# Kernel tuning notes

Measured on AMD Instinct MI355X. Metric: run time of the kernel, lower is better.

The kernel has to match this reference:

```python
import jax, jax.numpy as jnp
import numpy as np

HIDDEN_DIM = 512
SCALE = float(np.sqrt(HIDDEN_DIM))  # hidden_dim ** 0.5, matches torch


def setup_inputs() -> dict:
    key = jax.random.key(0)
    ks = jax.random.split(key, 4)
    B, S, D_IN = 8, 4096, 64
    x = jax.random.normal(ks[0], (B, S, D_IN), dtype=jnp.float32)
    # Linear weights stored as [in, out] (transposed vs torch's [out, in])
    Wq = jax.random.normal(ks[1], (D_IN, HIDDEN_DIM), dtype=jnp.float32) * (1.0 / np.sqrt(D_IN))
    Wk = jax.random.normal(ks[2], (D_IN, HIDDEN_DIM), dtype=jnp.float32) * (1.0 / np.sqrt(D_IN))
    Wv = jax.random.normal(ks[3], (D_IN, HIDDEN_DIM), dtype=jnp.float32) * (1.0 / np.sqrt(D_IN))
    bq = jnp.zeros((HIDDEN_DIM,), dtype=jnp.float32)
    bk = jnp.zeros((HIDDEN_DIM,), dtype=jnp.float32)
    bv = jnp.zeros((HIDDEN_DIM,), dtype=jnp.float32)
    return {"x": x, "Wq": Wq, "bq": bq, "Wk": Wk, "bk": bk, "Wv": Wv, "bv": bv}


def reference(x, Wq, bq, Wk, bk, Wv, bv):
    # Q/K/V projections: [B, S, H]
    Q = jnp.einsum('bsd,dh->bsh', x, Wq) + bq
    K = jnp.einsum('bsd,dh->bsh', x, Wk) + bk
    V = jnp.einsum('bsd,dh->bsh', x, Wv) + bv
    # Naive single-head attention with full [B, S, S] score matrix,
    # matching the original torch math exactly.
    scores = jnp.einsum('bqh,bkh->bqk', Q, K) / SCALE
    attn = jax.nn.softmax(scores, axis=-1)
    return jnp.einsum('bqk,bkh->bqh', attn, V)
```

## Files before the change

kernel.cpp:

```cpp
#include <hip/hip_runtime.h>
#include <hip/hip_bf16.h>
#include <math.h>


#define SS 4096
#define DD 64
#define HH 512

#define CSCALE ((float)(1.4426950408889634 * 0.04419417382415922))

typedef __bf16 bf16x8 __attribute__((ext_vector_type(8)));
typedef float  f32x4  __attribute__((ext_vector_type(4)));
typedef float  f32x16 __attribute__((ext_vector_type(16)));
typedef unsigned int u32x4 __attribute__((ext_vector_type(4)));

__device__ __forceinline__ float b2f(__hip_bfloat16 v) { return __bfloat162float(v); }

__device__ __forceinline__ f32x4 mfma16(bf16x8 a, bf16x8 b, f32x4 c) {
  return __builtin_amdgcn_mfma_f32_16x16x32_bf16(a, b, c, 0, 0, 0);
}
__device__ __forceinline__ f32x16 mfma32(bf16x8 a, bf16x8 b, f32x16 c) {
  return __builtin_amdgcn_mfma_f32_32x32x16_bf16(a, b, c, 0, 0, 0);
}

__device__ __forceinline__ unsigned pack2(float a, float b) {
  float2 f2; f2.x = a; f2.y = b;
  __hip_bfloat162 h2 = __float22bfloat162_rn(f2);
  unsigned u; __builtin_memcpy(&u, &h2, 4);
  return u;
}

__device__ __forceinline__ float loadf(const void* p, size_t i, int isF32) {
  return isF32 ? ((const float*)p)[i] : b2f(((const __hip_bfloat16*)p)[i]);
}
__device__ __forceinline__ void load8f(const void* p, size_t i, int isF32, float* o) {
  if (isF32) {
    const float4 a = *(const float4*)((const float*)p + i);
    const float4 b = *(const float4*)((const float*)p + i + 4);
    o[0]=a.x; o[1]=a.y; o[2]=a.z; o[3]=a.w; o[4]=b.x; o[5]=b.y; o[6]=b.z; o[7]=b.w;
  } else {
    const bf16x8 v = *(const bf16x8*)((const __hip_bfloat16*)p + i);
#pragma unroll
    for (int k = 0; k < 8; ++k) { __hip_bfloat16 h; __builtin_memcpy(&h, ((const unsigned short*)&v) + k, 2); o[k] = b2f(h); }
  }
}

__global__ void dtype_probe(const void* __restrict__ Wq, int* __restrict__ flag) {
  const unsigned short* h = (const unsigned short*)Wq;
  const int lane = threadIdx.x;
  unsigned int bits = ((unsigned int)h[lane * 2]) << 16;
  float v; __builtin_memcpy(&v, &bits, 4);
  v = fabsf(v);
  if (!isfinite(v) || v > 1e10f) v = 1e10f;
  for (int off = 1; off < 64; off <<= 1) v = fmaxf(v, __shfl_xor(v, off, 64));
  if (lane == 0) *flag = (v > 1e6f) ? 1 : 0;
}

__global__ __launch_bounds__(256) void prep_kernel(
    const void* __restrict__ Wq, const void* __restrict__ Wk,
    const void* __restrict__ Wv, const void* __restrict__ bq,
    const void* __restrict__ bk, __hip_bfloat16* __restrict__ MT,
    float* __restrict__ u, float* __restrict__ w_, float* __restrict__ c_,
    __hip_bfloat16* __restrict__ wvT, const int* __restrict__ flag) {
  const int t = threadIdx.x, blk = blockIdx.x;
  const int isF32 = *flag;
  if (blk < 64) {
    __shared__ float red[256];
    const int i = blk, j = t >> 2, part = t & 3;
    float acc = 0.f, aq[8], ak[8];
    for (int c = 0; c < 16; ++c) {
      load8f(Wq, (size_t)i * HH + part * 128 + c * 8, isF32, aq);
      load8f(Wk, (size_t)j * HH + part * 128 + c * 8, isF32, ak);
#pragma unroll
      for (int k = 0; k < 8; ++k) acc = fmaf(aq[k], ak[k], acc);
    }
    red[t] = acc;
    __syncthreads();
    if (t < 64)
      MT[t * 64 + i] = __float2bfloat16(red[t*4] + red[t*4+1] + red[t*4+2] + red[t*4+3]);
  } else if (blk == 64) {
    __shared__ float pu[256], pw[256], pc[64];
    const int i = t & 63, part = t >> 6;
    float au = 0.f, aw = 0.f, v1[8], v2[8];
    for (int c = 0; c < 16; ++c) {
      load8f(Wq, (size_t)i * HH + part * 128 + c * 8, isF32, v1);
      load8f(bk, part * 128 + c * 8, isF32, v2);
#pragma unroll
      for (int k = 0; k < 8; ++k) au = fmaf(v1[k], v2[k], au);
      load8f(Wk, (size_t)i * HH + part * 128 + c * 8, isF32, v1);
      load8f(bq, part * 128 + c * 8, isF32, v2);
#pragma unroll
      for (int k = 0; k < 8; ++k) aw = fmaf(v1[k], v2[k], aw);
    }
    pu[t] = au; pw[t] = aw;
    if (t < 64) {
      float s = 0.f;
      for (int e = 0; e < 8; ++e)
        s = fmaf(loadf(bq, t * 8 + e, isF32), loadf(bk, t * 8 + e, isF32), s);
      pc[t] = s;
    }
    __syncthreads();
    if (t < 64) {
      u[t]  = pu[t] + pu[t+64] + pu[t+128] + pu[t+192];
      w_[t] = pw[t] + pw[t+64] + pw[t+128] + pw[t+192];
    }
    if (t == 0) {
      float s = 0.f;
      for (int e = 0; e < 64; ++e) s += pc[e];
      *c_ = s;
    }
  } else {
    const int base = (blk - 65) * 2048 + t;
    for (int r = 0; r < 8; ++r) {
      const int e = base + r * 256;
      const int h = e >> 6, d = e & 63;
      wvT[e] = __float2bfloat16(loadf(Wv, (size_t)d * HH + h, isF32));
    }
  }
}

__global__ __launch_bounds__(256) void proj_kernel(
    const void* __restrict__ xraw, const __hip_bfloat16* __restrict__ MT,
    const float* __restrict__ u, const float* __restrict__ w_,
    const float* __restrict__ c_, __hip_bfloat16* __restrict__ xc,
    __hip_bfloat16* __restrict__ y, float* __restrict__ qb,
    float* __restrict__ kb, __hip_bfloat16* __restrict__ xT,
    const int* __restrict__ flag) {
  __shared__ __hip_bfloat16 xs[64 * 72];
  __shared__ __hip_bfloat16 Ms[64 * 72];
  __shared__ float us[64], wl[64];
  __shared__ float cs;

  const int t = threadIdx.x;
  const int isF32 = *flag;
  {
    const int r = t >> 2, cb = (t & 3) * 16;
    *(bf16x8*)(&Ms[r * 72 + cb])     = *(const bf16x8*)(MT + r * 64 + cb);
    *(bf16x8*)(&Ms[r * 72 + cb + 8]) = *(const bf16x8*)(MT + r * 64 + cb + 8);
  }
  if (t < 64) { us[t] = u[t]; wl[t] = w_[t]; }
  if (t == 0) cs = *c_;

  const int b = blockIdx.x & 7;
  const int sbase = (blockIdx.x >> 3) * 64;
  const int rbase = b * SS + sbase;

  for (int i = 0; i < 2; ++i) {
    const int e = i * 256 + t;
    const int row = e >> 3, col = (e & 7) * 8;
    float v[8];
    load8f(xraw, (size_t)(rbase + row) * DD + col, isF32, v);
    __hip_bfloat16* dp = xs + row * 72 + col;
#pragma unroll
    for (int k = 0; k < 8; ++k) dp[k] = __float2bfloat16(v[k]);
  }
  __syncthreads();

  const int wv = t >> 6, lane = t & 63;
  const int l16 = lane & 15, quad = lane >> 4;
  const bf16x8 A0 = *(const bf16x8*)(&xs[(wv * 16 + l16) * 72 + quad * 8]);
  const bf16x8 A1 = *(const bf16x8*)(&xs[(wv * 16 + l16) * 72 + 32 + quad * 8]);
#pragma unroll
  for (int nt = 0; nt < 4; ++nt) {
    const bf16x8 B0 = *(const bf16x8*)(&Ms[(nt * 16 + l16) * 72 + quad * 8]);
    const bf16x8 B1 = *(const bf16x8*)(&Ms[(nt * 16 + l16) * 72 + 32 + quad * 8]);
    f32x4 C = (f32x4){0.f, 0.f, 0.f, 0.f};
    C = mfma16(A0, B0, C);
    C = mfma16(A1, B1, C);
#pragma unroll
    for (int r = 0; r < 4; ++r)
      y[(size_t)(rbase + wv * 16 + quad * 4 + r) * DD + nt * 16 + l16] =
          __float2bfloat16(C[r]);
  }
  if (t < 64) {
    float qa = 0.f, ka = 0.f;
    for (int d = 0; d < 64; ++d) {
      const float xv = b2f(xs[t * 72 + d]);
      qa = fmaf(xv, us[d], qa);
      ka = fmaf(xv, wl[d], ka);
    }
    qb[rbase + t] = (qa + cs) * CSCALE;
    kb[rbase + t] = ka * CSCALE;
  }
  for (int i = 0; i < 2; ++i) {
    const int e = i * 256 + t;
    const int row = e >> 3, col = (e & 7) * 8;
    *(bf16x8*)(xc + (size_t)(rbase + row) * DD + col) = *(const bf16x8*)(xs + row * 72 + col);
  }
  for (int i = 0; i < 16; ++i) {
    const int d = i * 4 + (t >> 6);
    const int sl = t & 63;
    xT[((size_t)b * DD + d) * SS + sbase + sl] = xs[sl * 72 + d];
  }
}

__global__ __launch_bounds__(256) void attn_split(
    const __hip_bfloat16* __restrict__ x,
    const __hip_bfloat16* __restrict__ y,
    const float* __restrict__ qb, const float* __restrict__ kb,
    const __hip_bfloat16* __restrict__ xT,
    float* __restrict__ Opart, float* __restrict__ lpart, int lgs) {
  __shared__ __hip_bfloat16 xs[2][32 * 72];
  __shared__ __hip_bfloat16 vsm[2][64 * 40];
  const int tid = threadIdx.x;
  const int wv = tid >> 6, lane = tid & 63;
  const int l32 = lane & 31, hi = lane >> 5;
  const int b = blockIdx.x & 7;
  const int nspl = 1 << lgs;
  const int ks = (blockIdx.x >> 3) & (nspl - 1);
  const int qg = blockIdx.x >> (3 + lgs);
  const int kspl = SS >> lgs;
  const int koff = ks * kspl;
  const size_t rowq = ((size_t)b << 12) + (size_t)qg * 128 + wv * 32;

  bf16x8 Y[4];
#pragma unroll
  for (int mi = 0; mi < 4; ++mi)
    Y[mi] = *(const bf16x8*)(y + (rowq + l32) * DD + mi * 16 + hi * 8);
  const float qbl = qb[rowq + l32];

  const int sxr = tid >> 3, sxc = (tid & 7) * 8;
  const int g = sxr >> 2;
  const int taur = (sxr & 3) + 4 * ((g & 4) | ((g & 1) << 1) | ((g >> 1) & 1));
  const int svd = tid >> 2, svc = (tid & 3) * 8;
  const __hip_bfloat16* gx = x + ((size_t)b * SS + koff + sxr) * DD + sxc;
  const __hip_bfloat16* gv = xT + ((size_t)b * DD + svd) * SS + koff + svc;
  const float* kbp = kb + (size_t)b * SS + koff + hi * 8;

  bf16x8 nx = *(const bf16x8*)gx;
  bf16x8 nv = *(const bf16x8*)gv;
  *(bf16x8*)(&xs[0][taur * 72 + sxc]) = nx;
  *(bf16x8*)(&vsm[0][svd * 40 + svc]) = nv;
  nx = *(const bf16x8*)(gx + 32 * DD);
  nv = *(const bf16x8*)(gv + 32);
  __syncthreads();

  f32x16 O0, O1;
#pragma unroll
  for (int r = 0; r < 16; ++r) { O0[r] = 0.f; O1[r] = 0.f; }
  float lp = 0.f;

  for (int kt = 0; kt < kspl; kt += 32) {
    const int p = (kt >> 5) & 1, np = p ^ 1;
    if (kt + 32 < kspl) {
      *(bf16x8*)(&xs[np][taur * 72 + sxc]) = nx;
      *(bf16x8*)(&vsm[np][svd * 40 + svc]) = nv;
      if (kt + 64 < kspl) {
        nx = *(const bf16x8*)(gx + (size_t)(kt + 64) * DD);
        nv = *(const bf16x8*)(gv + (kt + 64));
      }
    }
    const f32x4 kb0a = *(const f32x4*)(kbp + kt);
    const f32x4 kb0b = *(const f32x4*)(kbp + kt + 4);
    const f32x4 kb1a = *(const f32x4*)(kbp + kt + 16);
    const f32x4 kb1b = *(const f32x4*)(kbp + kt + 20);

    const bf16x8 A0 = *(const bf16x8*)(&xs[p][l32 * 72 + hi * 8]);
    const bf16x8 A1 = *(const bf16x8*)(&xs[p][l32 * 72 + 16 + hi * 8]);
    const bf16x8 A2 = *(const bf16x8*)(&xs[p][l32 * 72 + 32 + hi * 8]);
    const bf16x8 A3 = *(const bf16x8*)(&xs[p][l32 * 72 + 48 + hi * 8]);

    f32x16 S;
#pragma unroll
    for (int r = 0; r < 16; ++r) S[r] = 0.f;
    S = mfma32(A0, Y[0], S);
    S = mfma32(A1, Y[1], S);
    S = mfma32(A2, Y[2], S);
    S = mfma32(A3, Y[3], S);

    float pv[16];
#pragma unroll
    for (int r = 0; r < 16; ++r) {
      const float kv = (r < 4) ? kb0a[r & 3]
                     : (r < 8) ? kb0b[r & 3]
                     : (r < 12) ? kb1a[r & 3] : kb1b[r & 3];
      pv[r] = __builtin_amdgcn_exp2f(fmaf(S[r], CSCALE, qbl + kv));
    }
    {
      float s0 = (pv[0]+pv[1]) + (pv[2]+pv[3]);
      float s1 = (pv[4]+pv[5]) + (pv[6]+pv[7]);
      float s2 = (pv[8]+pv[9]) + (pv[10]+pv[11]);
      float s3 = (pv[12]+pv[13]) + (pv[14]+pv[15]);
      lp += (s0 + s1) + (s2 + s3);
    }
    u32x4 R0, R1;
    R0[0] = pack2(pv[0], pv[1]);  R0[1] = pack2(pv[2], pv[3]);
    R0[2] = pack2(pv[4], pv[5]);  R0[3] = pack2(pv[6], pv[7]);
    R1[0] = pack2(pv[8], pv[9]);  R1[1] = pack2(pv[10], pv[11]);
    R1[2] = pack2(pv[12], pv[13]); R1[3] = pack2(pv[14], pv[15]);
    bf16x8 Pf0, Pf1;
    __builtin_memcpy(&Pf0, &R0, 16);
    __builtin_memcpy(&Pf1, &R1, 16);

    const bf16x8 V00 = *(const bf16x8*)(&vsm[p][l32 * 40 + hi * 8]);
    const bf16x8 V10 = *(const bf16x8*)(&vsm[p][l32 * 40 + 16 + hi * 8]);
    const bf16x8 V01 = *(const bf16x8*)(&vsm[p][(l32 + 32) * 40 + hi * 8]);
    const bf16x8 V11 = *(const bf16x8*)(&vsm[p][(l32 + 32) * 40 + 16 + hi * 8]);

    O0 = mfma32(Pf0, V00, O0);
    O0 = mfma32(Pf1, V10, O0);
    O1 = mfma32(Pf0, V01, O1);
    O1 = mfma32(Pf1, V11, O1);

    __syncthreads();
  }

  lp += __shfl_xor(lp, 32, 64);
  const size_t NP = (size_t)SS * 8;
  if (hi == 0) lpart[(size_t)ks * NP + rowq + l32] = lp;

  float* Op = Opart + ((size_t)ks * NP + rowq) * 64;
#pragma unroll
  for (int r = 0; r < 16; ++r) {
    const int qrow = (r & 3) + 8 * (r >> 2) + 4 * hi;
    Op[(size_t)qrow * 64 + l32]      = O0[r];
    Op[(size_t)qrow * 64 + 32 + l32] = O1[r];
  }
}

__global__ __launch_bounds__(128) void combine_kernel(
    const float* __restrict__ Opart, const float* __restrict__ lpart,
    const __hip_bfloat16* __restrict__ wvT, const void* __restrict__ bv_raw,
    void* __restrict__ out_raw, const int* __restrict__ flag, int nspl) {
  const int tid = threadIdx.x;
  const int wv = tid >> 6, lane = tid & 63;
  const int l16 = lane & 15, quad = lane >> 4;
  const size_t q0 = (size_t)blockIdx.x * 32 + (size_t)wv * 16;
  const int isF32 = *flag;
  const size_t NP = (size_t)SS * 8;

  float lsum = 0.f;
  for (int s = 0; s < nspl; ++s) lsum += lpart[(size_t)s * NP + q0 + l16];
  const float linv = (lsum > 0.f) ? 1.0f / lsum : 0.f;

  float vlo[8], vhi[8];
#pragma unroll
  for (int j = 0; j < 8; ++j) { vlo[j] = 0.f; vhi[j] = 0.f; }
  for (int s = 0; s < nspl; ++s) {
    const float* p0 = Opart + ((size_t)s * NP + q0 + l16) * 64 + quad * 8;
#pragma unroll
    for (int j = 0; j < 8; j += 4) {
      const float4 a = *(const float4*)(p0 + j);
      vlo[j]   += a.x; vlo[j+1] += a.y; vlo[j+2] += a.z; vlo[j+3] += a.w;
      const float4 c = *(const float4*)(p0 + 32 + j);
      vhi[j]   += c.x; vhi[j+1] += c.y; vhi[j+2] += c.z; vhi[j+3] += c.w;
    }
  }
  u32x4 Rlo, Rhi;
#pragma unroll
  for (int j = 0; j < 4; ++j) {
    Rlo[j] = pack2(vlo[2*j] * linv, vlo[2*j+1] * linv);
    Rhi[j] = pack2(vhi[2*j] * linv, vhi[2*j+1] * linv);
  }
  bf16x8 Alo, Ahi;
  __builtin_memcpy(&Alo, &Rlo, 16);
  __builtin_memcpy(&Ahi, &Rhi, 16);

  float* outf = (float*)out_raw;
  __hip_bfloat16* outb = (__hip_bfloat16*)out_raw;
#pragma unroll 4
  for (int ht = 0; ht < 32; ++ht) {
    const __hip_bfloat16* wp = wvT + (size_t)(ht * 16 + l16) * DD + quad * 8;
    const bf16x8 Wlo = *(const bf16x8*)wp;
    const bf16x8 Whi = *(const bf16x8*)(wp + 32);
    f32x4 C = (f32x4){0.f, 0.f, 0.f, 0.f};
    C = mfma16(Alo, Wlo, C);
    C = mfma16(Ahi, Whi, C);
    const float bvv = loadf(bv_raw, ht * 16 + l16, isF32);
#pragma unroll
    for (int r = 0; r < 4; ++r) {
      const size_t oidx = (q0 + quad * 4 + r) * HH + ht * 16 + l16;
      const float val = C[r] + bvv;
      if (isF32) outf[oidx] = val;
      else       outb[oidx] = __float2bfloat16(val);
    }
  }
}

__global__ __launch_bounds__(256) void attn_kernel(
    const __hip_bfloat16* __restrict__ x,
    const __hip_bfloat16* __restrict__ y,
    const float* __restrict__ qb, const float* __restrict__ kb,
    const __hip_bfloat16* __restrict__ xT,
    const __hip_bfloat16* __restrict__ wvT,
    const void* __restrict__ bv_raw,
    void* __restrict__ out_raw, const int* __restrict__ flag) {
  __shared__ __hip_bfloat16 xs[2][32 * 72];
  __shared__ __hip_bfloat16 vsm[2][64 * 40];
  __shared__ float kbl[SS];
  const int tid = threadIdx.x;
  const int wv = tid >> 6, lane = tid & 63;
  const int l16 = lane & 15, quad = lane >> 4;
  const int b = blockIdx.x & 7;
  const int qt = (blockIdx.x >> 3) * 4 + wv;
  const size_t rowq = ((size_t)b << 12) + ((size_t)qt << 4);
  const int isF32 = *flag;

  const __hip_bfloat16* xb  = x  + ((size_t)b * SS) * DD;
  const __hip_bfloat16* xTb = xT + ((size_t)b * DD) * SS;
  const float* kbb = kb + ((size_t)b * SS);

  const __hip_bfloat16* yp = y + (rowq + l16) * DD + quad * 8;
  const bf16x8 Ylo = *(const bf16x8*)yp;
  const bf16x8 Yhi = *(const bf16x8*)(yp + 32);
  const float qbl = qb[rowq + l16];

  const int sxr = tid >> 3, sxc = (tid & 7) * 8;
  const int taur = (sxr & 3) + ((sxr >> 3) << 2) + (((sxr >> 2) & 1) << 4);
  const int svd = tid >> 2, svc = (tid & 3) * 8;
  const __hip_bfloat16* gx = xb + (size_t)sxr * DD + sxc;
  const __hip_bfloat16* gv = xTb + (size_t)svd * SS + svc;

#pragma unroll
  for (int j = 0; j < 4; ++j) {
    const int c = j * 256 + tid;
    *(f32x4*)(&kbl[c * 4]) = *(const f32x4*)(kbb + c * 4);
  }

  bf16x8 nx = *(const bf16x8*)gx;
  bf16x8 nv = *(const bf16x8*)gv;
  *(bf16x8*)(&xs[0][taur * 72 + sxc]) = nx;
  *(bf16x8*)(&vsm[0][svd * 40 + svc]) = nv;
  nx = *(const bf16x8*)(gx + 32 * DD);
  nv = *(const bf16x8*)(gv + 32);
  __syncthreads();

  bf16x8 onesb;
#pragma unroll
  for (int j = 0; j < 8; ++j) onesb[j] = (__bf16)1.0f;

  f32x4 O[4];
#pragma unroll
  for (int n = 0; n < 4; ++n) O[n] = (f32x4){0.f, 0.f, 0.f, 0.f};
  f32x4 Ol = (f32x4){0.f, 0.f, 0.f, 0.f};

  for (int kt = 0; kt < SS; kt += 32) {
    const int p = (kt >> 5) & 1, np = p ^ 1;
    if (kt + 32 < SS) {
      *(bf16x8*)(&xs[np][taur * 72 + sxc]) = nx;
      *(bf16x8*)(&vsm[np][svd * 40 + svc]) = nv;
      if (kt + 64 < SS) {
        nx = *(const bf16x8*)(gx + (size_t)(kt + 64) * DD);
        nv = *(const bf16x8*)(gv + (kt + 64));
      }
    }
    const bf16x8 B00 = *(const bf16x8*)(&xs[p][l16 * 72 + quad * 8]);
    const bf16x8 B01 = *(const bf16x8*)(&xs[p][l16 * 72 + 32 + quad * 8]);
    const bf16x8 B10 = *(const bf16x8*)(&xs[p][(16 + l16) * 72 + quad * 8]);
    const bf16x8 B11 = *(const bf16x8*)(&xs[p][(16 + l16) * 72 + 32 + quad * 8]);
    const bf16x8 V0 = *(const bf16x8*)(&vsm[p][l16 * 40 + quad * 8]);
    const bf16x8 V1 = *(const bf16x8*)(&vsm[p][(16 + l16) * 40 + quad * 8]);
    const bf16x8 V2 = *(const bf16x8*)(&vsm[p][(32 + l16) * 40 + quad * 8]);
    const bf16x8 V3 = *(const bf16x8*)(&vsm[p][(48 + l16) * 40 + quad * 8]);

    f32x4 S0 = (f32x4){0.f, 0.f, 0.f, 0.f};
    f32x4 S1 = (f32x4){0.f, 0.f, 0.f, 0.f};
    S0 = mfma16(B00, Ylo, S0);
    S0 = mfma16(B01, Yhi, S0);
    S1 = mfma16(B10, Ylo, S1);
    S1 = mfma16(B11, Yhi, S1);

    const f32x4 kb0 = *(const f32x4*)(&kbl[kt + quad * 8]);
    const f32x4 kb1 = *(const f32x4*)(&kbl[kt + quad * 8 + 4]);

    float p0[4], p1[4];
#pragma unroll
    for (int r = 0; r < 4; ++r) {
      p0[r] = __builtin_amdgcn_exp2f(fmaf(S0[r], CSCALE, qbl + kb0[r]));
      p1[r] = __builtin_amdgcn_exp2f(fmaf(S1[r], CSCALE, qbl + kb1[r]));
    }
    u32x4 R;
    R[0] = pack2(p0[0], p0[1]);
    R[1] = pack2(p0[2], p0[3]);
    R[2] = pack2(p1[0], p1[1]);
    R[3] = pack2(p1[2], p1[3]);
    bf16x8 Pf;
    __builtin_memcpy(&Pf, &R, 16);

    O[0] = mfma16(Pf, V0, O[0]);
    O[1] = mfma16(Pf, V1, O[1]);
    O[2] = mfma16(Pf, V2, O[2]);
    O[3] = mfma16(Pf, V3, O[3]);
    Ol = mfma16(Pf, onesb, Ol);

    __syncthreads();
  }

  float inv_l[4];
#pragma unroll
  for (int r = 0; r < 4; ++r)
    inv_l[r] = (Ol[r] > 0.f) ? 1.0f / Ol[r] : 0.f;
  __hip_bfloat16* pl = &xs[0][0] + wv * 1152;
#pragma unroll
  for (int n = 0; n < 4; ++n)
#pragma unroll
    for (int r = 0; r < 4; ++r) {
      const int row = quad * 4 + r;
      pl[row * 72 + n * 16 + l16] = __float2bfloat16(O[n][r] * inv_l[r]);
    }
  __syncthreads();
  const bf16x8 Alo = *(const bf16x8*)(pl + l16 * 72 + quad * 8);
  const bf16x8 Ahi = *(const bf16x8*)(pl + l16 * 72 + 32 + quad * 8);

  float* outf = (float*)out_raw;
  __hip_bfloat16* outb = (__hip_bfloat16*)out_raw;
#pragma unroll 4
  for (int ht = 0; ht < 32; ++ht) {
    const __hip_bfloat16* wp = wvT + (size_t)(ht * 16 + l16) * DD + quad * 8;
    const bf16x8 Wlo = *(const bf16x8*)wp;
    const bf16x8 Whi = *(const bf16x8*)(wp + 32);
    f32x4 C = (f32x4){0.f, 0.f, 0.f, 0.f};
    C = mfma16(Alo, Wlo, C);
    C = mfma16(Ahi, Whi, C);
    const float bvv = loadf(bv_raw, ht * 16 + l16, isF32);
#pragma unroll
    for (int r = 0; r < 4; ++r) {
      const size_t oidx = (rowq + quad * 4 + r) * HH + ht * 16 + l16;
      const float val = C[r] + bvv;
      if (isF32) outf[oidx] = val;
      else       outb[oidx] = __float2bfloat16(val);
    }
  }
}

extern "C" void kernel_launch(void* const* d_in, const int* in_sizes, int n_in,
                              void* d_out, int out_size, void* d_ws,
                              size_t ws_size, hipStream_t stream) {
  char* ws = (char*)d_ws;
  int*   flag = (int*)(ws + 0);
  __hip_bfloat16* MT = (__hip_bfloat16*)(ws + 1024);
  float* u    = (float*)(ws + 9216);
  float* w_   = (float*)(ws + 9728);
  float* c_   = (float*)(ws + 10240);
  __hip_bfloat16* wvT = (__hip_bfloat16*)(ws + 32768);
  __hip_bfloat16* xc  = (__hip_bfloat16*)(ws + 131072);
  __hip_bfloat16* y   = (__hip_bfloat16*)(ws + 4325376);
  float* qb = (float*)(ws + 8519680);
  float* kb = (float*)(ws + 8650752);
  __hip_bfloat16* xT = (__hip_bfloat16*)(ws + 8781824);
  float* Opart = (float*)(ws + 16777216);
  const size_t NP = (size_t)SS * 8;
  const size_t need4 = 16777216UL + 4UL * NP * 64 * 4 + 4UL * NP * 4;
  const size_t need2 = 16777216UL + 2UL * NP * 64 * 4 + 2UL * NP * 4;

  dtype_probe<<<1, 64, 0, stream>>>(d_in[1], flag);
  prep_kernel<<<81, 256, 0, stream>>>(d_in[1], d_in[3], d_in[5], d_in[2],
                                      d_in[4], MT, u, w_, c_, wvT, flag);
  proj_kernel<<<512, 256, 0, stream>>>(d_in[0], MT, u, w_, c_, xc, y, qb, kb,
                                       xT, flag);
  if (ws_size >= need4) {
    float* lpart = (float*)(ws + 16777216 + 4UL * NP * 64 * 4);
    attn_split<<<1024, 256, 0, stream>>>(xc, y, qb, kb, xT, Opart, lpart, 2);
    combine_kernel<<<1024, 128, 0, stream>>>(Opart, lpart, wvT, d_in[6], d_out,
                                             flag, 4);
  } else if (ws_size >= need2) {
    float* lpart = (float*)(ws + 16777216 + 2UL * NP * 64 * 4);
    attn_split<<<512, 256, 0, stream>>>(xc, y, qb, kb, xT, Opart, lpart, 1);
    combine_kernel<<<1024, 128, 0, stream>>>(Opart, lpart, wvT, d_in[6], d_out,
                                             flag, 2);
  } else {
    attn_kernel<<<512, 256, 0, stream>>>(xc, y, qb, kb, xT, wvT, d_in[6],
                                         d_out, flag);
  }
}
```

Baseline: 193.0 us.

## Fuse split-K combine and V projection into attention via last-block atomic counter

Replaces the separate combine kernel with a last-arriving-block scheme inside the split attention kernel. Each query group's four key-split blocks bump an atomic counter, and the last one sums the partial O and l values, normalizes them, and runs the Wv projection with bias straight to the output. The counters are zeroed in proj_kernel. This removes a kernel launch and its tail, but leaves the final projection to only a quarter of the blocks and adds fences and atomics.

```diff
diff --git a/kernel.cpp b/kernel.cpp
--- a/kernel.cpp
+++ b/kernel.cpp
@@ -125,7 +125,7 @@
     const float* __restrict__ c_, __hip_bfloat16* __restrict__ xc,
     __hip_bfloat16* __restrict__ y, float* __restrict__ qb,
     float* __restrict__ kb, __hip_bfloat16* __restrict__ xT,
-    const int* __restrict__ flag) {
+    int* __restrict__ cnt, const int* __restrict__ flag) {
   __shared__ __hip_bfloat16 xs[64 * 72];
   __shared__ __hip_bfloat16 Ms[64 * 72];
   __shared__ float us[64], wl[64];
@@ -133,6 +133,7 @@
 
   const int t = threadIdx.x;
   const int isF32 = *flag;
+  if (blockIdx.x == 0 && t < 256) cnt[t] = 0;
   {
     const int r = t >> 2, cb = (t & 3) * 16;
     *(bf16x8*)(&Ms[r * 72 + cb])     = *(const bf16x8*)(MT + r * 64 + cb);
@@ -191,6 +192,196 @@
     const int d = i * 4 + (t >> 6);
     const int sl = t & 63;
     xT[((size_t)b * DD + d) * SS + sbase + sl] = xs[sl * 72 + d];
+  }
+}
+
+__global__ __launch_bounds__(256) void attn_split_fused(
+    const __hip_bfloat16* __restrict__ x,
+    const __hip_bfloat16* __restrict__ y,
+    const float* __restrict__ qb, const float* __restrict__ kb,
+    const __hip_bfloat16* __restrict__ xT,
+    float* __restrict__ Opart, float* __restrict__ lpart,
+    int* __restrict__ cnt,
+    const __hip_bfloat16* __restrict__ wvT, const void* __restrict__ bv_raw,
+    void* __restrict__ out_raw, const int* __restrict__ flag) {
+  __shared__ __hip_bfloat16 xs[2][32 * 72];
+  __shared__ __hip_bfloat16 vsm[2][64 * 40];
+  __shared__ int lastflag;
+  const int tid = threadIdx.x;
+  const int wv = tid >> 6, lane = tid & 63;
+  const int l32 = lane & 31, hi = lane >> 5;
+  const int b = blockIdx.x & 7;
+  const int ks = (blockIdx.x >> 3) & 3;
+  const int qg = blockIdx.x >> 5;
+  const int kspl = SS >> 2;
+  const int koff = ks * kspl;
+  const size_t rowq = ((size_t)b << 12) + ((size_t)(qg & 31)) * 128 + wv * 32;
+  const size_t NP = (size_t)SS * 8;
+
+  bf16x8 Y[4];
+#pragma unroll
+  for (int mi = 0; mi < 4; ++mi)
+    Y[mi] = *(const bf16x8*)(y + (rowq + l32) * DD + mi * 16 + hi * 8);
+  const float qbl = qb[rowq + l32];
+
+  const int sxr = tid >> 3, sxc = (tid & 7) * 8;
+  const int g = sxr >> 2;
+  const int taur = (sxr & 3) + 4 * ((g & 4) | ((g & 1) << 1) | ((g >> 1) & 1));
+  const int svd = tid >> 2, svc = (tid & 3) * 8;
+  const __hip_bfloat16* gx = x + ((size_t)b * SS + koff + sxr) * DD + sxc;
+  const __hip_bfloat16* gv = xT + ((size_t)b * DD + svd) * SS + koff + svc;
+  const float* kbp = kb + (size_t)b * SS + koff + hi * 8;
+
+  bf16x8 nx = *(const bf16x8*)gx;
+  bf16x8 nv = *(const bf16x8*)gv;
+  *(bf16x8*)(&xs[0][taur * 72 + sxc]) = nx;
+  *(bf16x8*)(&vsm[0][svd * 40 + svc]) = nv;
+  nx = *(const bf16x8*)(gx + 32 * DD);
+  nv = *(const bf16x8*)(gv + 32);
+  __syncthreads();
+
+  f32x16 O0, O1;
+#pragma unroll
+  for (int r = 0; r < 16; ++r) { O0[r] = 0.f; O1[r] = 0.f; }
+  float lp = 0.f;
+
+  for (int kt = 0; kt < kspl; kt += 32) {
+    const int p = (kt >> 5) & 1, np = p ^ 1;
+    if (kt + 32 < kspl) {
+      *(bf16x8*)(&xs[np][taur * 72 + sxc]) = nx;
+      *(bf16x8*)(&vsm[np][svd * 40 + svc]) = nv;
+      if (kt + 64 < kspl) {
+        nx = *(const bf16x8*)(gx + (size_t)(kt + 64) * DD);
+        nv = *(const bf16x8*)(gv + (kt + 64));
+      }
+    }
+    const f32x4 kb0a = *(const f32x4*)(kbp + kt);
+    const f32x4 kb0b = *(const f32x4*)(kbp + kt + 4);
+    const f32x4 kb1a = *(const f32x4*)(kbp + kt + 16);
+    const f32x4 kb1b = *(const f32x4*)(kbp + kt + 20);
+
+    const bf16x8 A0 = *(const bf16x8*)(&xs[p][l32 * 72 + hi * 8]);
+    const bf16x8 A1 = *(const bf16x8*)(&xs[p][l32 * 72 + 16 + hi * 8]);
+    const bf16x8 A2 = *(const bf16x8*)(&xs[p][l32 * 72 + 32 + hi * 8]);
+    const bf16x8 A3 = *(const bf16x8*)(&xs[p][l32 * 72 + 48 + hi * 8]);
+
+    f32x16 S;
+#pragma unroll
+    for (int r = 0; r < 16; ++r) S[r] = 0.f;
+    S = mfma32(A0, Y[0], S);
+    S = mfma32(A1, Y[1], S);
+    S = mfma32(A2, Y[2], S);
+    S = mfma32(A3, Y[3], S);
+
+    float pv[16];
+#pragma unroll
+    for (int r = 0; r < 16; ++r) {
+      const float kv = (r < 4) ? kb0a[r & 3]
+                     : (r < 8) ? kb0b[r & 3]
+                     : (r < 12) ? kb1a[r & 3] : kb1b[r & 3];
+      pv[r] = __builtin_amdgcn_exp2f(fmaf(S[r], CSCALE, qbl + kv));
+    }
+    {
+      float s0 = (pv[0]+pv[1]) + (pv[2]+pv[3]);
+      float s1 = (pv[4]+pv[5]) + (pv[6]+pv[7]);
+      float s2 = (pv[8]+pv[9]) + (pv[10]+pv[11]);
+      float s3 = (pv[12]+pv[13]) + (pv[14]+pv[15]);
+      lp += (s0 + s1) + (s2 + s3);
+    }
+    u32x4 R0, R1;
+    R0[0] = pack2(pv[0], pv[1]);  R0[1] = pack2(pv[2], pv[3]);
+    R0[2] = pack2(pv[4], pv[5]);  R0[3] = pack2(pv[6], pv[7]);
+    R1[0] = pack2(pv[8], pv[9]);  R1[1] = pack2(pv[10], pv[11]);
+    R1[2] = pack2(pv[12], pv[13]); R1[3] = pack2(pv[14], pv[15]);
+    bf16x8 Pf0, Pf1;
+    __builtin_memcpy(&Pf0, &R0, 16);
+    __builtin_memcpy(&Pf1, &R1, 16);
+
+    const bf16x8 V00 = *(const bf16x8*)(&vsm[p][l32 * 40 + hi * 8]);
+    const bf16x8 V10 = *(const bf16x8*)(&vsm[p][l32 * 40 + 16 + hi * 8]);
+    const bf16x8 V01 = *(const bf16x8*)(&vsm[p][(l32 + 32) * 40 + hi * 8]);
+    const bf16x8 V11 = *(const bf16x8*)(&vsm[p][(l32 + 32) * 40 + 16 + hi * 8]);
+
+    O0 = mfma32(Pf0, V00, O0);
+    O0 = mfma32(Pf1, V10, O0);
+    O1 = mfma32(Pf0, V01, O1);
+    O1 = mfma32(Pf1, V11, O1);
+
+    __syncthreads();
+  }
+
+  lp += __shfl_xor(lp, 32, 64);
+  if (hi == 0) lpart[(size_t)ks * NP + rowq + l32] = lp;
+
+  float* Op = Opart + ((size_t)ks * NP + rowq) * 64;
+#pragma unroll
+  for (int r = 0; r < 16; ++r) {
+    const int qrow = (r & 3) + 8 * (r >> 2) + 4 * hi;
+    Op[(size_t)qrow * 64 + l32]      = O0[r];
+    Op[(size_t)qrow * 64 + 32 + l32] = O1[r];
+  }
+
+  __syncthreads();
+  if (tid == 0) {
+    __threadfence();
+    const int gid = b * 32 + (int)(qg & 31);
+    const int old = atomicAdd(&cnt[gid], 1);
+    lastflag = (old == 3);
+  }
+  __syncthreads();
+  if (!lastflag) return;
+  __threadfence();
+
+  const int isF32 = *flag;
+  float lsum = 0.f;
+#pragma unroll
+  for (int s = 0; s < 4; ++s) lsum += lpart[(size_t)s * NP + rowq + l32];
+  const float linv = (lsum > 0.f) ? 1.0f / lsum : 0.f;
+
+  bf16x8 PA[4];
+  const float* Ob = Opart + rowq * 64;
+#pragma unroll
+  for (int mi = 0; mi < 4; ++mi) {
+    const int dbase = mi * 16 + hi * 8;
+    float acc[8];
+#pragma unroll
+    for (int j = 0; j < 8; ++j) acc[j] = 0.f;
+#pragma unroll
+    for (int s = 0; s < 4; ++s) {
+      const float* pp = Ob + (size_t)s * NP * 64 + (size_t)l32 * 64 + dbase;
+      const float4 a = *(const float4*)pp;
+      const float4 c = *(const float4*)(pp + 4);
+      acc[0] += a.x; acc[1] += a.y; acc[2] += a.z; acc[3] += a.w;
+      acc[4] += c.x; acc[5] += c.y; acc[6] += c.z; acc[7] += c.w;
+    }
+    u32x4 R;
+#pragma unroll
+    for (int j = 0; j < 4; ++j)
+      R[j] = pack2(acc[2*j] * linv, acc[2*j+1] * linv);
+    __builtin_memcpy(&PA[mi], &R, 16);
+  }
+
+  float* outf = (float*)out_raw;
+  __hip_bfloat16* outb = (__hip_bfloat16*)out_raw;
+  for (int nt = 0; nt < 16; ++nt) {
+    const int h = nt * 32 + l32;
+    f32x16 C;
+#pragma unroll
+    for (int r = 0; r < 16; ++r) C[r] = 0.f;
+#pragma unroll
+    for (int mi = 0; mi < 4; ++mi) {
+      const bf16x8 Bf = *(const bf16x8*)(wvT + (size_t)h * DD + mi * 16 + hi * 8);
+      C = mfma32(PA[mi], Bf, C);
+    }
+    const float bvv = loadf(bv_raw, h, isF32);
+#pragma unroll
+    for (int r = 0; r < 16; ++r) {
+      const int qrow = (r & 3) + 8 * (r >> 2) + 4 * hi;
+      const size_t oidx = (rowq + qrow) * HH + h;
+      const float val = C[r] + bvv;
+      if (isF32) outf[oidx] = val;
+      else       outb[oidx] = __float2bfloat16(val);
+    }
   }
 }
 
@@ -532,6 +723,7 @@
   float* u    = (float*)(ws + 9216);
   float* w_   = (float*)(ws + 9728);
   float* c_   = (float*)(ws + 10240);
+  int*   cnt  = (int*)(ws + 12288);
   __hip_bfloat16* wvT = (__hip_bfloat16*)(ws + 32768);
   __hip_bfloat16* xc  = (__hip_bfloat16*)(ws + 131072);
   __hip_bfloat16* y   = (__hip_bfloat16*)(ws + 4325376);
@@ -547,12 +739,12 @@
   prep_kernel<<<81, 256, 0, stream>>>(d_in[1], d_in[3], d_in[5], d_in[2],
                                       d_in[4], MT, u, w_, c_, wvT, flag);
   proj_kernel<<<512, 256, 0, stream>>>(d_in[0], MT, u, w_, c_, xc, y, qb, kb,
-                                       xT, flag);
+                                       xT, cnt, flag);
   if (ws_size >= need4) {
     float* lpart = (float*)(ws + 16777216 + 4UL * NP * 64 * 4);
-    attn_split<<<1024, 256, 0, stream>>>(xc, y, qb, kb, xT, Opart, lpart, 2);
-    combine_kernel<<<1024, 128, 0, stream>>>(Opart, lpart, wvT, d_in[6], d_out,
-                                             flag, 4);
+    attn_split_fused<<<1024, 256, 0, stream>>>(xc, y, qb, kb, xT, Opart,
+                                               lpart, cnt, wvT, d_in[6],
+                                               d_out, flag);
   } else if (ws_size >= need2) {
     float* lpart = (float*)(ws + 16777216 + 2UL * NP * 64 * 4);
     attn_split<<<512, 256, 0, stream>>>(xc, y, qb, kb, xT, Opart, lpart, 1);
```

Result: slower. 267.7 us (+38.7%).
